# Kernel optimization log

Hardware: AMD Instinct MI355X
Metric: run time of the kernel (lower is better)

The kernel has to match this reference:

```python
import jax, jax.numpy as jnp
import numpy as np

N, E, F_IN, HID, HEADS, OUT, EDIM = 50000, 800000, 128, 64, 2, 40, 5
NEG_SLOPE = 0.2


def setup_inputs() -> dict:
    key = jax.random.key(0)
    ks = jax.random.split(key, 16)
    x = jax.random.normal(ks[0], (N, F_IN), jnp.float32)
    # build edge_index with src != dst so PyG's remove_self_loops is a no-op
    dst = jax.random.randint(ks[1], (E,), 0, N, dtype=jnp.int32)
    off = jax.random.randint(ks[2], (E,), 1, N, dtype=jnp.int32)
    src = (dst + off) % N
    edge_index = jnp.stack([src, dst], axis=0)
    edge_attr = jax.random.normal(ks[3], (E, EDIM), jnp.float32)
    s = 0.1
    params = dict(
        W1=jax.random.normal(ks[4], (F_IN, HEADS * HID), jnp.float32) * s,
        att_src1=jax.random.normal(ks[5], (HEADS, HID), jnp.float32) * s,
        att_dst1=jax.random.normal(ks[6], (HEADS, HID), jnp.float32) * s,
        We1=jax.random.normal(ks[7], (EDIM, HEADS * HID), jnp.float32) * s,
        att_e1=jax.random.normal(ks[8], (HEADS, HID), jnp.float32) * s,
        b1=jnp.zeros((HEADS * HID,), jnp.float32),
        W2=jax.random.normal(ks[9], (HEADS * HID, OUT), jnp.float32) * s,
        att_src2=jax.random.normal(ks[10], (1, OUT), jnp.float32) * s,
        att_dst2=jax.random.normal(ks[11], (1, OUT), jnp.float32) * s,
        We2=jax.random.normal(ks[12], (EDIM, OUT), jnp.float32) * s,
        att_e2=jax.random.normal(ks[13], (1, OUT), jnp.float32) * s,
        b2=jnp.zeros((OUT,), jnp.float32),
    )
    return dict(x=x, edge_index=edge_index, edge_attr=edge_attr, **params)


def _add_self_loops(src, dst, eattr, n):
    # PyG add_self_loops with fill_value='mean': per-dst-node mean of incoming edge_attr
    cnt = jax.ops.segment_sum(jnp.ones_like(dst, jnp.float32), dst, num_segments=n)
    loop_attr = jax.ops.segment_sum(eattr, dst, num_segments=n) / jnp.maximum(cnt, 1.0)[:, None]
    ar = jnp.arange(n, dtype=src.dtype)
    return (jnp.concatenate([src, ar]), jnp.concatenate([dst, ar]),
            jnp.concatenate([eattr, loop_attr], axis=0))


def _gat_conv(x, src, dst, eattr, W, a_src, a_dst, We, a_e, b):
    n = x.shape[0]
    H, C = a_src.shape
    xh = (x @ W).reshape(n, H, C)                      # [N,H,C]
    al_src = jnp.einsum('nhc,hc->nh', xh, a_src)[src]  # [Etot,H]
    al_dst = jnp.einsum('nhc,hc->nh', xh, a_dst)[dst]
    eh = (eattr @ We).reshape(-1, H, C)                # [Etot,H,C]
    al_e = jnp.einsum('ehc,hc->eh', eh, a_e)
    alpha = jax.nn.leaky_relu(al_src + al_dst + al_e, negative_slope=NEG_SLOPE)
    amax = jax.ops.segment_max(alpha, dst, num_segments=n)  # segment-wise softmax over dst
    ex = jnp.exp(alpha - amax[dst])
    denom = jax.ops.segment_sum(ex, dst, num_segments=n)
    alpha = ex / (denom[dst] + 1e-16)
    out = jax.ops.segment_sum(xh[src] * alpha[:, :, None], dst, num_segments=n)
    return out.reshape(n, H * C) + b


def reference(x, edge_index, edge_attr, W1, att_src1, att_dst1, We1, att_e1, b1,
              W2, att_src2, att_dst2, We2, att_e2, b2):
    src, dst = edge_index[0], edge_index[1]
    s2, d2, ea2 = _add_self_loops(src, dst, edge_attr, x.shape[0])
    h = jax.nn.elu(_gat_conv(x, s2, d2, ea2, W1, att_src1, att_dst1, We1, att_e1, b1))
    logits = _gat_conv(h, s2, d2, ea2, W2, att_src2, att_dst2, We2, att_e2, b2)
    return jax.nn.log_softmax(logits, axis=1)
```

## Files before the change

### kernel.cpp

```cpp
#include <hip/hip_runtime.h>
#include <hip/hip_fp16.h>
#include <math.h>

#define N_NODES 50000
#define N_EDGES 800000
#define F_IN    128
#define HID     64
#define HEADS   2
#define C1      128
#define OUT_C   40
#define EDIM    5
#define NEG_SLOPE 0.2f
#define CAPN    64
#define NPB1    16
#define NPB2    8
#define SCAN_B  256
#define SCAN_NB ((N_NODES + SCAN_B - 1) / SCAN_B)

constexpr size_t pad64(size_t n){ return (n + 63) / 64 * 64; }
constexpr size_t O_CNT      = 0;
constexpr size_t O_ZERO_END = O_CNT      + pad64(N_NODES);
constexpr size_t O_RANK     = O_ZERO_END;
constexpr size_t O_ROWPTR   = O_RANK     + pad64(N_EDGES);
constexpr size_t O_STMP     = O_ROWPTR   + pad64(N_NODES+1);
constexpr size_t O_BSUM     = O_STMP     + pad64(N_NODES);
constexpr size_t O_BOFF     = O_BSUM     + pad64(SCAN_NB);
constexpr size_t O_EREC     = O_BOFF     + pad64(SCAN_NB);
constexpr size_t O_WEATT    = O_EREC     + pad64((size_t)N_EDGES*2);
constexpr size_t O_XHB      = O_WEATT    + 64;
constexpr size_t O_AS1      = O_XHB      + pad64((size_t)N_NODES*C1/2);
constexpr size_t O_AD1      = O_AS1      + pad64((size_t)N_NODES*2);
constexpr size_t O_H1       = O_AD1      + pad64((size_t)N_NODES*2);
constexpr size_t O_XH2B     = O_H1       + pad64((size_t)N_NODES*C1);
constexpr size_t O_AS2      = O_XH2B     + pad64((size_t)N_NODES*OUT_C/2);
constexpr size_t O_AD2      = O_AS2      + pad64(N_NODES);

__device__ __forceinline__ float lrelu(float v){ return v >= 0.f ? v : NEG_SLOPE*v; }
__device__ __forceinline__ float bfl(unsigned u){ return __uint_as_float(u << 16); }
__device__ __forceinline__ float bfh(unsigned u){ return __uint_as_float(u & 0xFFFF0000u); }
__device__ __forceinline__ unsigned short f2bf(float f){
  unsigned u = __float_as_uint(f);
  return (unsigned short)((u + 0x7FFFu + ((u >> 16) & 1u)) >> 16);
}
__device__ __forceinline__ unsigned f2h(float f){
  return (unsigned)__half_as_ushort(__float2half(f));
}
__device__ __forceinline__ float h2f(unsigned u){
  return __half2float(__ushort_as_half((unsigned short)(u & 0xFFFFu)));
}

__global__ void k_weatt(const float* __restrict__ We1, const float* __restrict__ ae1,
                        const float* __restrict__ We2, const float* __restrict__ ae2,
                        float* __restrict__ weatt){
  int t = threadIdx.x;
  if (t < 10){
    int k = t >> 1, h = t & 1;
    float s = 0.f;
    for (int c = 0; c < HID; c++) s += We1[k*C1 + h*HID + c] * ae1[h*HID + c];
    weatt[k*2 + h] = s;
  } else if (t < 15){
    int k = t - 10;
    float s = 0.f;
    for (int c = 0; c < OUT_C; c++) s += We2[k*OUT_C + c] * ae2[c];
    weatt[10 + k] = s;
  }
}

__global__ void k_count(const int* __restrict__ dst, int* __restrict__ cnt,
                        int* __restrict__ rank){
  int e = blockIdx.x*blockDim.x + threadIdx.x;
  if (e >= N_EDGES) return;
  rank[e] = atomicAdd(&cnt[dst[e]], 1);
}

__global__ void __launch_bounds__(SCAN_B) k_scan1(const int* __restrict__ cnt,
                                                  int* __restrict__ stmp,
                                                  int* __restrict__ bsum){
  int blk = blockIdx.x, t = threadIdx.x;
  int i = blk*SCAN_B + t;
  int v = (i < N_NODES) ? cnt[i] : 0;
  int lane = t & 63, w = t >> 6;
  int x = v;
  #pragma unroll
  for (int off = 1; off < 64; off <<= 1){
    int y = __shfl_up(x, off);
    if (lane >= off) x += y;
  }
  __shared__ int wsum[SCAN_B/64];
  if (lane == 63) wsum[w] = x;
  __syncthreads();
  int add = 0;
  for (int k = 0; k < w; k++) add += wsum[k];
  x += add;
  if (i < N_NODES) stmp[i] = x;
  if (t == SCAN_B-1) bsum[blk] = x;
}

__global__ void __launch_bounds__(SCAN_B) k_scan2(const int* __restrict__ bsum,
                                                  int* __restrict__ boff){
  int t = threadIdx.x;
  int v = (t < SCAN_NB) ? bsum[t] : 0;
  int lane = t & 63, w = t >> 6;
  int x = v;
  #pragma unroll
  for (int off = 1; off < 64; off <<= 1){
    int y = __shfl_up(x, off);
    if (lane >= off) x += y;
  }
  __shared__ int wsum[SCAN_B/64];
  if (lane == 63) wsum[w] = x;
  __syncthreads();
  int add = 0;
  for (int k = 0; k < w; k++) add += wsum[k];
  x += add;
  if (t < SCAN_NB) boff[t] = x - v;
}

__global__ void __launch_bounds__(SCAN_B) k_scan3(const int* __restrict__ stmp,
                                                  const int* __restrict__ boff,
                                                  int* __restrict__ rowptr){
  int blk = blockIdx.x, t = threadIdx.x;
  int i = blk*SCAN_B + t;
  if (i < N_NODES) rowptr[i+1] = stmp[i] + boff[blk];
  if (i == 0) rowptr[0] = 0;
}

__global__ void k_scatter(const int* __restrict__ src, const int* __restrict__ dst,
                          const int* __restrict__ rank,
                          const float* __restrict__ eattr, const int* __restrict__ rowptr,
                          const float* __restrict__ weatt,
                          uint2* __restrict__ erec){
  int e = blockIdx.x*blockDim.x + threadIdx.x;
  if (e >= N_EDGES) return;
  int d = dst[e];
  int pos = rowptr[d] + rank[e];
  float a[EDIM];
  #pragma unroll
  for (int k = 0; k < EDIM; k++) a[k] = eattr[e*EDIM + k];
  float l0 = 0.f, l1 = 0.f, l2 = 0.f;
  #pragma unroll
  for (int k = 0; k < EDIM; k++){
    l0 += a[k]*weatt[k*2 + 0];
    l1 += a[k]*weatt[k*2 + 1];
    l2 += a[k]*weatt[10 + k];
  }
  unsigned w0 = (unsigned)src[e] | (f2h(l2) << 16);
  unsigned w1 = f2h(l0) | (f2h(l1) << 16);
  erec[pos] = make_uint2(w0, w1);
}

#define T1_ROWS 128
#define T1_KK   32
__global__ void __launch_bounds__(256) k_gemm1(const float* __restrict__ x,
                                               const float* __restrict__ W,
                                               const float* __restrict__ a_src,
                                               const float* __restrict__ a_dst,
                                               unsigned short* __restrict__ xhb,
                                               float* __restrict__ as_o,
                                               float* __restrict__ ad_o){
  __shared__ float xs[T1_ROWS][T1_KK+1];
  __shared__ float ws[T1_KK][C1];
  int tid = threadIdx.x;
  int tx = tid & 15, ty = tid >> 4;
  int r0 = blockIdx.x * T1_ROWS;
  float acc[8][8];
  #pragma unroll
  for (int i = 0; i < 8; i++)
    #pragma unroll
    for (int j = 0; j < 8; j++) acc[i][j] = 0.f;

  for (int kb = 0; kb < F_IN; kb += T1_KK){
    __syncthreads();
    for (int i = tid; i < T1_ROWS*(T1_KK/4); i += 256){
      int r = i >> 3, c4 = (i & 7) * 4;
      int row = r0 + r;
      float4 v = (row < N_NODES) ? *(const float4*)&x[(size_t)row*F_IN + kb + c4]
                                 : make_float4(0.f,0.f,0.f,0.f);
      xs[r][c4+0]=v.x; xs[r][c4+1]=v.y; xs[r][c4+2]=v.z; xs[r][c4+3]=v.w;
    }
    for (int i = tid; i < T1_KK*(C1/4); i += 256){
      int k = i >> 5, c4 = (i & 31) * 4;
      *(float4*)&ws[k][c4] = *(const float4*)&W[(size_t)(kb + k)*C1 + c4];
    }
    __syncthreads();
    #pragma unroll 4
    for (int k = 0; k < T1_KK; k++){
      float a[8], b[8];
      #pragma unroll
      for (int i = 0; i < 8; i++) a[i] = xs[ty*8 + i][k];
      float4 b0 = *(const float4*)&ws[k][tx*8];
      float4 b1 = *(const float4*)&ws[k][tx*8+4];
      b[0]=b0.x; b[1]=b0.y; b[2]=b0.z; b[3]=b0.w;
      b[4]=b1.x; b[5]=b1.y; b[6]=b1.z; b[7]=b1.w;
      #pragma unroll
      for (int i = 0; i < 8; i++)
        #pragma unroll
        for (int j = 0; j < 8; j++)
          acc[i][j] += a[i]*b[j];
    }
  }
  float asv[8], adv[8];
  #pragma unroll
  for (int j = 0; j < 8; j++){
    asv[j] = a_src[tx*8 + j];
    adv[j] = a_dst[tx*8 + j];
  }
  int h = tx >> 3;
  #pragma unroll
  for (int i = 0; i < 8; i++){
    int row = r0 + ty*8 + i;
    bool ok = row < N_NODES;
    if (ok){
      unsigned short hh[8];
      #pragma unroll
      for (int j = 0; j < 8; j++) hh[j] = f2bf(acc[i][j]);
      uint4 pk;
      pk.x = (unsigned)hh[0] | ((unsigned)hh[1] << 16);
      pk.y = (unsigned)hh[2] | ((unsigned)hh[3] << 16);
      pk.z = (unsigned)hh[4] | ((unsigned)hh[5] << 16);
      pk.w = (unsigned)hh[6] | ((unsigned)hh[7] << 16);
      *(uint4*)&xhb[(size_t)row*C1 + tx*8] = pk;
    }
    float s = 0.f, d = 0.f;
    #pragma unroll
    for (int j = 0; j < 8; j++){ s += acc[i][j]*asv[j]; d += acc[i][j]*adv[j]; }
    s += __shfl_xor(s, 1); s += __shfl_xor(s, 2); s += __shfl_xor(s, 4);
    d += __shfl_xor(d, 1); d += __shfl_xor(d, 2); d += __shfl_xor(d, 4);
    if (ok && (tx & 7) == 0){
      as_o[row*2 + h] = s;
      ad_o[row*2 + h] = d;
    }
  }
}

__global__ void __launch_bounds__(256) k_agg1(const unsigned short* __restrict__ xhb,
    const int* __restrict__ rowptr, const uint2* __restrict__ erec,
    const float* __restrict__ as1, const float* __restrict__ ad1,
    const float* __restrict__ b1, float* __restrict__ h1){
  __shared__ float2 eC[NPB1][CAPN+1];
  __shared__ int    sC[NPB1][CAPN+1];
  int t = threadIdx.x;
  int g = t >> 4, l = t & 15;
  int n = blockIdx.x*NPB1 + g;
  if (n >= N_NODES) return;
  int beg = rowptr[n], end = rowptr[n+1];
  int deg = end - beg;
  float2 adn = *(const float2*)&ad1[n*2];
  bool cached = (deg <= CAPN);

  float s0 = 0.f, s1 = 0.f, la0 = 0.f, la1 = 0.f;
  for (int i = l; i < deg; i += 16){
    uint2 r = erec[(size_t)beg + i];
    int s = r.x & 0xFFFFu;
    float al0 = h2f(r.y), al1 = h2f(r.y >> 16);
    float2 a = *(const float2*)&as1[s*2];
    float e0 = expf(lrelu(a.x + adn.x + al0));
    float e1 = expf(lrelu(a.y + adn.y + al1));
    if (cached){ sC[g][i] = s * C1; eC[g][i] = make_float2(e0, e1); }
    s0 += e0; s1 += e1; la0 += al0; la1 += al1;
  }
  #pragma unroll
  for (int off = 1; off < 16; off <<= 1){
    s0 += __shfl_xor(s0, off); s1 += __shfl_xor(s1, off);
    la0 += __shfl_xor(la0, off); la1 += __shfl_xor(la1, off);
  }
  float inv = 1.f / fmaxf((float)deg, 1.f);
  float2 asn = *(const float2*)&as1[n*2];
  float sl0 = lrelu(asn.x + adn.x + la0*inv);
  float sl1 = lrelu(asn.y + adn.y + la1*inv);
  float es0 = expf(sl0), es1 = expf(sl1);
  float S0 = s0 + es0 + 1e-16f;
  float S1 = s1 + es1 + 1e-16f;

  int head = l >> 3;
  float acc[8];
  #pragma unroll
  for (int j = 0; j < 8; j++) acc[j] = 0.f;
  if (cached){
    for (int k = 0; k < deg; k++){
      float2 e2 = eC[g][k];
      float e = head ? e2.y : e2.x;
      uint4 r = *(const uint4*)&xhb[sC[g][k] + l*8];
      acc[0] += e*bfl(r.x); acc[1] += e*bfh(r.x);
      acc[2] += e*bfl(r.y); acc[3] += e*bfh(r.y);
      acc[4] += e*bfl(r.z); acc[5] += e*bfh(r.z);
      acc[6] += e*bfl(r.w); acc[7] += e*bfh(r.w);
    }
  } else {
    for (int k = 0; k < deg; k++){
      uint2 rr = erec[(size_t)beg + k];
      int s = rr.x & 0xFFFFu;
      float2 a = *(const float2*)&as1[s*2];
      float e = head ? expf(lrelu(a.y + adn.y + h2f(rr.y >> 16)))
                     : expf(lrelu(a.x + adn.x + h2f(rr.y)));
      uint4 r = *(const uint4*)&xhb[(size_t)s*C1 + l*8];
      acc[0] += e*bfl(r.x); acc[1] += e*bfh(r.x);
      acc[2] += e*bfl(r.y); acc[3] += e*bfh(r.y);
      acc[4] += e*bfl(r.z); acc[5] += e*bfh(r.z);
      acc[6] += e*bfl(r.w); acc[7] += e*bfh(r.w);
    }
  }
  float es = head ? es1 : es0;
  float den = head ? S1 : S0;
  uint4 r = *(const uint4*)&xhb[(size_t)n*C1 + l*8];
  float xs8[8];
  xs8[0]=bfl(r.x); xs8[1]=bfh(r.x); xs8[2]=bfl(r.y); xs8[3]=bfh(r.y);
  xs8[4]=bfl(r.z); xs8[5]=bfh(r.z); xs8[6]=bfl(r.w); xs8[7]=bfh(r.w);
  float o[8];
  #pragma unroll
  for (int j = 0; j < 8; j++){
    float v = (acc[j] + es*xs8[j]) / den + b1[l*8 + j];
    o[j] = v > 0.f ? v : expm1f(v);
  }
  *(float4*)&h1[(size_t)n*C1 + l*8]     = make_float4(o[0],o[1],o[2],o[3]);
  *(float4*)&h1[(size_t)n*C1 + l*8 + 4] = make_float4(o[4],o[5],o[6],o[7]);
}

#define T2_ROWS 128
#define T2_KK   32
__global__ void __launch_bounds__(256) k_gemm2(const float* __restrict__ h1,
    const float* __restrict__ W2, const float* __restrict__ a_src2,
    const float* __restrict__ a_dst2,
    unsigned short* __restrict__ xh2b, float* __restrict__ as_o, float* __restrict__ ad_o){
  __shared__ float hs[T2_ROWS][T2_KK+1];
  __shared__ float ws[F_IN*OUT_C];
  int tid = threadIdx.x;
  int tx = tid & 7, ty = tid >> 3;
  int r0 = blockIdx.x * T2_ROWS;
  for (int i = tid; i < F_IN*OUT_C/4; i += 256)
    ((float4*)ws)[i] = ((const float4*)W2)[i];
  float acc[4][5];
  #pragma unroll
  for (int i = 0; i < 4; i++)
    #pragma unroll
    for (int j = 0; j < 5; j++) acc[i][j] = 0.f;

  for (int kb = 0; kb < F_IN; kb += T2_KK){
    __syncthreads();
    for (int i = tid; i < T2_ROWS*(T2_KK/4); i += 256){
      int r = i >> 3, c4 = (i & 7) * 4;
      int row = r0 + r;
      float4 v = (row < N_NODES) ? *(const float4*)&h1[(size_t)row*F_IN + kb + c4]
                                 : make_float4(0.f,0.f,0.f,0.f);
      hs[r][c4+0]=v.x; hs[r][c4+1]=v.y; hs[r][c4+2]=v.z; hs[r][c4+3]=v.w;
    }
    __syncthreads();
    #pragma unroll 4
    for (int k = 0; k < T2_KK; k++){
      float a[4], b[5];
      #pragma unroll
      for (int i = 0; i < 4; i++) a[i] = hs[ty*4 + i][k];
      #pragma unroll
      for (int j = 0; j < 5; j++) b[j] = ws[(kb + k)*OUT_C + tx*5 + j];
      #pragma unroll
      for (int i = 0; i < 4; i++)
        #pragma unroll
        for (int j = 0; j < 5; j++)
          acc[i][j] += a[i]*b[j];
    }
  }
  float asv[5], adv[5];
  #pragma unroll
  for (int j = 0; j < 5; j++){
    asv[j] = a_src2[tx*5 + j];
    adv[j] = a_dst2[tx*5 + j];
  }
  #pragma unroll
  for (int i = 0; i < 4; i++){
    int row = r0 + ty*4 + i;
    bool ok = row < N_NODES;
    if (ok){
      #pragma unroll
      for (int j = 0; j < 5; j++)
        xh2b[(size_t)row*OUT_C + tx*5 + j] = f2bf(acc[i][j]);
    }
    float s = 0.f, d = 0.f;
    #pragma unroll
    for (int j = 0; j < 5; j++){ s += acc[i][j]*asv[j]; d += acc[i][j]*adv[j]; }
    s += __shfl_xor(s, 1); s += __shfl_xor(s, 2); s += __shfl_xor(s, 4);
    d += __shfl_xor(d, 1); d += __shfl_xor(d, 2); d += __shfl_xor(d, 4);
    if (ok && tx == 0){
      as_o[row] = s;
      ad_o[row] = d;
    }
  }
}

__global__ void __launch_bounds__(256) k_agg2(const unsigned short* __restrict__ xh2b,
    const int* __restrict__ rowptr, const uint2* __restrict__ erec,
    const float* __restrict__ as2, const float* __restrict__ ad2,
    const float* __restrict__ b2, float* __restrict__ out){
  __shared__ float eC[NPB2][CAPN+1];
  __shared__ int   sC[NPB2][CAPN+1];
  int t = threadIdx.x;
  int g = t >> 5, l = t & 31;
  int n = blockIdx.x*NPB2 + g;
  if (n >= N_NODES) return;
  int beg = rowptr[n], end = rowptr[n+1];
  int deg = end - beg;
  float adv = ad2[n];
  bool cached = (deg <= CAPN);

  float ss = 0.f, la = 0.f;
  for (int i = l; i < deg; i += 32){
    uint2 r = erec[(size_t)beg + i];
    int s = r.x & 0xFFFFu;
    float al2 = h2f(r.x >> 16);
    float e = expf(lrelu(as2[s] + adv + al2));
    if (cached){ sC[g][i] = s * OUT_C; eC[g][i] = e; }
    ss += e; la += al2;
  }
  #pragma unroll
  for (int off = 1; off < 32; off <<= 1){
    ss += __shfl_xor(ss, off);
    la += __shfl_xor(la, off);
  }
  float inv = 1.f / fmaxf((float)deg, 1.f);
  float sl = lrelu(as2[n] + adv + la*inv);
  float es = expf(sl);
  float S = ss + es + 1e-16f;

  float a0 = 0.f, a1 = 0.f;
  if (l < 20){
    if (cached){
      for (int k = 0; k < deg; k++){
        float e = eC[g][k];
        unsigned u = *(const unsigned*)&xh2b[sC[g][k] + l*2];
        a0 += e*bfl(u); a1 += e*bfh(u);
      }
    } else {
      for (int k = 0; k < deg; k++){
        uint2 rr = erec[(size_t)beg + k];
        int s = rr.x & 0xFFFFu;
        float e = expf(lrelu(as2[s] + adv + h2f(rr.x >> 16)));
        unsigned u = *(const unsigned*)&xh2b[(size_t)s*OUT_C + l*2];
        a0 += e*bfl(u); a1 += e*bfh(u);
      }
    }
  }
  float o0 = -INFINITY, o1 = -INFINITY;
  if (l < 20){
    unsigned u = *(const unsigned*)&xh2b[(size_t)n*OUT_C + l*2];
    o0 = (a0 + es*bfl(u)) / S + b2[l*2 + 0];
    o1 = (a1 + es*bfh(u)) / S + b2[l*2 + 1];
  }
  float mm = fmaxf(o0, o1);
  #pragma unroll
  for (int off = 1; off < 32; off <<= 1) mm = fmaxf(mm, __shfl_xor(mm, off));
  float e = (l < 20) ? (expf(o0 - mm) + expf(o1 - mm)) : 0.f;
  #pragma unroll
  for (int off = 1; off < 32; off <<= 1) e += __shfl_xor(e, off);
  if (l < 20){
    float lse = logf(e);
    out[(size_t)n*OUT_C + l*2 + 0] = o0 - mm - lse;
    out[(size_t)n*OUT_C + l*2 + 1] = o1 - mm - lse;
  }
}

extern "C" void kernel_launch(void* const* d_in, const int* in_sizes, int n_in,
                              void* d_out, int out_size, void* d_ws, size_t ws_size,
                              hipStream_t stream){
  const float* x        = (const float*)d_in[0];
  const int*   ei       = (const int*)  d_in[1];
  const float* eattr    = (const float*)d_in[2];
  const float* W1       = (const float*)d_in[3];
  const float* att_src1 = (const float*)d_in[4];
  const float* att_dst1 = (const float*)d_in[5];
  const float* We1      = (const float*)d_in[6];
  const float* att_e1   = (const float*)d_in[7];
  const float* b1       = (const float*)d_in[8];
  const float* W2       = (const float*)d_in[9];
  const float* att_src2 = (const float*)d_in[10];
  const float* att_dst2 = (const float*)d_in[11];
  const float* We2      = (const float*)d_in[12];
  const float* att_e2   = (const float*)d_in[13];
  const float* b2       = (const float*)d_in[14];
  const int* src = ei;
  const int* dst = ei + N_EDGES;

  float* wsf    = (float*)d_ws;
  int*   cnt     = (int*)(wsf + O_CNT);
  int*   rank    = (int*)(wsf + O_RANK);
  int*   rowptr  = (int*)(wsf + O_ROWPTR);
  int*   stmp    = (int*)(wsf + O_STMP);
  int*   bsum    = (int*)(wsf + O_BSUM);
  int*   boff    = (int*)(wsf + O_BOFF);
  uint2* erec    = (uint2*)(wsf + O_EREC);
  float* weatt   = wsf + O_WEATT;
  unsigned short* xhb  = (unsigned short*)(wsf + O_XHB);
  float* as1     = wsf + O_AS1;
  float* ad1     = wsf + O_AD1;
  float* h1      = wsf + O_H1;
  unsigned short* xh2b = (unsigned short*)(wsf + O_XH2B);
  float* as2     = wsf + O_AS2;
  float* ad2     = wsf + O_AD2;
  float* out     = (float*)d_out;

  hipMemsetAsync(wsf + O_CNT, 0, O_ZERO_END*sizeof(float), stream);

  const int EB = (N_EDGES + 255) / 256;

  k_weatt  <<<1, 64, 0, stream>>>(We1, att_e1, We2, att_e2, weatt);
  k_count  <<<EB, 256, 0, stream>>>(dst, cnt, rank);
  k_scan1  <<<SCAN_NB, SCAN_B, 0, stream>>>(cnt, stmp, bsum);
  k_scan2  <<<1, SCAN_B, 0, stream>>>(bsum, boff);
  k_scan3  <<<SCAN_NB, SCAN_B, 0, stream>>>(stmp, boff, rowptr);
  k_scatter<<<EB, 256, 0, stream>>>(src, dst, rank, eattr, rowptr, weatt, erec);

  k_gemm1  <<<(N_NODES + T1_ROWS - 1)/T1_ROWS, 256, 0, stream>>>(x, W1, att_src1, att_dst1,
                                                                 xhb, as1, ad1);
  k_agg1   <<<(N_NODES + NPB1 - 1)/NPB1, 256, 0, stream>>>(xhb, rowptr, erec, as1, ad1, b1, h1);

  k_gemm2  <<<(N_NODES + T2_ROWS - 1)/T2_ROWS, 256, 0, stream>>>(h1, W2, att_src2, att_dst2,
                                                                 xh2b, as2, ad2);
  k_agg2   <<<(N_NODES + NPB2 - 1)/NPB2, 256, 0, stream>>>(xh2b, rowptr, erec, as2, ad2, b2, out);
}
```

Before: 190.6 us.

## Rewrite first-layer GEMM with bf16 MFMA and fold weatt into scan2

Replaces the FP32 register-tiled x@W1 kernel with a bf16 MFMA 16x16x32 kernel. Each block transposes all of W1 into LDS as bf16, each wave computes a 16x128 tile, and results are staged through LDS to pack bf16 output and compute the attention dot products. Separately, the tiny edge-attention weight precompute is merged into the single-block scan2 kernel to drop one launch. Converting x and W to bf16 before the multiply lowers accuracy relative to the FP32 accumulate path. Every block also re-converts the full 128x128 W1 into LDS.

```diff
diff --git a/kernel.cpp b/kernel.cpp
--- a/kernel.cpp
+++ b/kernel.cpp
@@ -16,6 +16,9 @@
 #define NPB2    8
 #define SCAN_B  256
 #define SCAN_NB ((N_NODES + SCAN_B - 1) / SCAN_B)
+
+typedef __bf16 bf16x8 __attribute__((ext_vector_type(8)));
+typedef float  f32x4v __attribute__((ext_vector_type(4)));
 
 constexpr size_t pad64(size_t n){ return (n + 63) / 64 * 64; }
 constexpr size_t O_CNT      = 0;
@@ -49,10 +52,59 @@
   return __half2float(__ushort_as_half((unsigned short)(u & 0xFFFFu)));
 }
 
-__global__ void k_weatt(const float* __restrict__ We1, const float* __restrict__ ae1,
-                        const float* __restrict__ We2, const float* __restrict__ ae2,
-                        float* __restrict__ weatt){
+__global__ void k_count(const int* __restrict__ dst, int* __restrict__ cnt,
+                        int* __restrict__ rank){
+  int e = blockIdx.x*blockDim.x + threadIdx.x;
+  if (e >= N_EDGES) return;
+  rank[e] = atomicAdd(&cnt[dst[e]], 1);
+}
+
+__global__ void __launch_bounds__(SCAN_B) k_scan1(const int* __restrict__ cnt,
+                                                  int* __restrict__ stmp,
+                                                  int* __restrict__ bsum){
+  int blk = blockIdx.x, t = threadIdx.x;
+  int i = blk*SCAN_B + t;
+  int v = (i < N_NODES) ? cnt[i] : 0;
+  int lane = t & 63, w = t >> 6;
+  int x = v;
+  #pragma unroll
+  for (int off = 1; off < 64; off <<= 1){
+    int y = __shfl_up(x, off);
+    if (lane >= off) x += y;
+  }
+  __shared__ int wsum[SCAN_B/64];
+  if (lane == 63) wsum[w] = x;
+  __syncthreads();
+  int add = 0;
+  for (int k = 0; k < w; k++) add += wsum[k];
+  x += add;
+  if (i < N_NODES) stmp[i] = x;
+  if (t == SCAN_B-1) bsum[blk] = x;
+}
+
+__global__ void __launch_bounds__(SCAN_B) k_scan2(const int* __restrict__ bsum,
+                                                  int* __restrict__ boff,
+                                                  const float* __restrict__ We1,
+                                                  const float* __restrict__ ae1,
+                                                  const float* __restrict__ We2,
+                                                  const float* __restrict__ ae2,
+                                                  float* __restrict__ weatt){
   int t = threadIdx.x;
+  int v = (t < SCAN_NB) ? bsum[t] : 0;
+  int lane = t & 63, w = t >> 6;
+  int x = v;
+  #pragma unroll
+  for (int off = 1; off < 64; off <<= 1){
+    int y = __shfl_up(x, off);
+    if (lane >= off) x += y;
+  }
+  __shared__ int wsum[SCAN_B/64];
+  if (lane == 63) wsum[w] = x;
+  __syncthreads();
+  int add = 0;
+  for (int k = 0; k < w; k++) add += wsum[k];
+  x += add;
+  if (t < SCAN_NB) boff[t] = x - v;
   if (t < 10){
     int k = t >> 1, h = t & 1;
     float s = 0.f;
@@ -66,56 +118,6 @@
   }
 }
 
-__global__ void k_count(const int* __restrict__ dst, int* __restrict__ cnt,
-                        int* __restrict__ rank){
-  int e = blockIdx.x*blockDim.x + threadIdx.x;
-  if (e >= N_EDGES) return;
-  rank[e] = atomicAdd(&cnt[dst[e]], 1);
-}
-
-__global__ void __launch_bounds__(SCAN_B) k_scan1(const int* __restrict__ cnt,
-                                                  int* __restrict__ stmp,
-                                                  int* __restrict__ bsum){
-  int blk = blockIdx.x, t = threadIdx.x;
-  int i = blk*SCAN_B + t;
-  int v = (i < N_NODES) ? cnt[i] : 0;
-  int lane = t & 63, w = t >> 6;
-  int x = v;
-  #pragma unroll
-  for (int off = 1; off < 64; off <<= 1){
-    int y = __shfl_up(x, off);
-    if (lane >= off) x += y;
-  }
-  __shared__ int wsum[SCAN_B/64];
-  if (lane == 63) wsum[w] = x;
-  __syncthreads();
-  int add = 0;
-  for (int k = 0; k < w; k++) add += wsum[k];
-  x += add;
-  if (i < N_NODES) stmp[i] = x;
-  if (t == SCAN_B-1) bsum[blk] = x;
-}
-
-__global__ void __launch_bounds__(SCAN_B) k_scan2(const int* __restrict__ bsum,
-                                                  int* __restrict__ boff){
-  int t = threadIdx.x;
-  int v = (t < SCAN_NB) ? bsum[t] : 0;
-  int lane = t & 63, w = t >> 6;
-  int x = v;
-  #pragma unroll
-  for (int off = 1; off < 64; off <<= 1){
-    int y = __shfl_up(x, off);
-    if (lane >= off) x += y;
-  }
-  __shared__ int wsum[SCAN_B/64];
-  if (lane == 63) wsum[w] = x;
-  __syncthreads();
-  int add = 0;
-  for (int k = 0; k < w; k++) add += wsum[k];
-  x += add;
-  if (t < SCAN_NB) boff[t] = x - v;
-}
-
 __global__ void __launch_bounds__(SCAN_B) k_scan3(const int* __restrict__ stmp,
                                                   const int* __restrict__ boff,
                                                   int* __restrict__ rowptr){
@@ -149,8 +151,6 @@
   erec[pos] = make_uint2(w0, w1);
 }
 
-#define T1_ROWS 128
-#define T1_KK   32
 __global__ void __launch_bounds__(256) k_gemm1(const float* __restrict__ x,
                                                const float* __restrict__ W,
                                                const float* __restrict__ a_src,
@@ -158,78 +158,83 @@
                                                unsigned short* __restrict__ xhb,
                                                float* __restrict__ as_o,
                                                float* __restrict__ ad_o){
-  __shared__ float xs[T1_ROWS][T1_KK+1];
-  __shared__ float ws[T1_KK][C1];
+  __shared__ __align__(16) unsigned char smem[128*136*2];
+  __bf16 (*wt)[136] = (__bf16(*)[136])smem;
+  float  (*eps)[132] = (float(*)[132])smem;
   int tid = threadIdx.x;
-  int tx = tid & 15, ty = tid >> 4;
-  int r0 = blockIdx.x * T1_ROWS;
-  float acc[8][8];
-  #pragma unroll
-  for (int i = 0; i < 8; i++)
+  int wv = tid >> 6, L = tid & 63;
+  int g = L >> 4, c16 = L & 15;
+  int r0 = blockIdx.x * 64;
+
+  for (int i = tid; i < F_IN*C1; i += 256){
+    int k = i >> 7, c = i & 127;
+    wt[c][k] = (__bf16)W[i];
+  }
+  __syncthreads();
+
+  f32x4v acc[8];
+  #pragma unroll
+  for (int ct = 0; ct < 8; ct++) acc[ct] = (f32x4v){0.f, 0.f, 0.f, 0.f};
+
+  int arow = r0 + wv*16 + c16;
+  bool aok = arow < N_NODES;
+  const float* xrow = &x[(size_t)arow*F_IN];
+  #pragma unroll
+  for (int ks = 0; ks < 4; ks++){
+    int k0 = ks*32 + g*8;
+    bf16x8 a;
+    if (aok){
+      float4 v0 = *(const float4*)&xrow[k0];
+      float4 v1 = *(const float4*)&xrow[k0 + 4];
+      a[0]=(__bf16)v0.x; a[1]=(__bf16)v0.y; a[2]=(__bf16)v0.z; a[3]=(__bf16)v0.w;
+      a[4]=(__bf16)v1.x; a[5]=(__bf16)v1.y; a[6]=(__bf16)v1.z; a[7]=(__bf16)v1.w;
+    } else {
+      a = (bf16x8)(__bf16)0.f;
+    }
     #pragma unroll
-    for (int j = 0; j < 8; j++) acc[i][j] = 0.f;
-
-  for (int kb = 0; kb < F_IN; kb += T1_KK){
-    __syncthreads();
-    for (int i = tid; i < T1_ROWS*(T1_KK/4); i += 256){
-      int r = i >> 3, c4 = (i & 7) * 4;
-      int row = r0 + r;
-      float4 v = (row < N_NODES) ? *(const float4*)&x[(size_t)row*F_IN + kb + c4]
-                                 : make_float4(0.f,0.f,0.f,0.f);
-      xs[r][c4+0]=v.x; xs[r][c4+1]=v.y; xs[r][c4+2]=v.z; xs[r][c4+3]=v.w;
-    }
-    for (int i = tid; i < T1_KK*(C1/4); i += 256){
-      int k = i >> 5, c4 = (i & 31) * 4;
-      *(float4*)&ws[k][c4] = *(const float4*)&W[(size_t)(kb + k)*C1 + c4];
-    }
-    __syncthreads();
-    #pragma unroll 4
-    for (int k = 0; k < T1_KK; k++){
-      float a[8], b[8];
-      #pragma unroll
-      for (int i = 0; i < 8; i++) a[i] = xs[ty*8 + i][k];
-      float4 b0 = *(const float4*)&ws[k][tx*8];
-      float4 b1 = *(const float4*)&ws[k][tx*8+4];
-      b[0]=b0.x; b[1]=b0.y; b[2]=b0.z; b[3]=b0.w;
-      b[4]=b1.x; b[5]=b1.y; b[6]=b1.z; b[7]=b1.w;
-      #pragma unroll
-      for (int i = 0; i < 8; i++)
-        #pragma unroll
-        for (int j = 0; j < 8; j++)
-          acc[i][j] += a[i]*b[j];
-    }
-  }
-  float asv[8], adv[8];
-  #pragma unroll
-  for (int j = 0; j < 8; j++){
-    asv[j] = a_src[tx*8 + j];
-    adv[j] = a_dst[tx*8 + j];
-  }
-  int h = tx >> 3;
-  #pragma unroll
-  for (int i = 0; i < 8; i++){
-    int row = r0 + ty*8 + i;
-    bool ok = row < N_NODES;
-    if (ok){
-      unsigned short hh[8];
-      #pragma unroll
-      for (int j = 0; j < 8; j++) hh[j] = f2bf(acc[i][j]);
-      uint4 pk;
-      pk.x = (unsigned)hh[0] | ((unsigned)hh[1] << 16);
-      pk.y = (unsigned)hh[2] | ((unsigned)hh[3] << 16);
-      pk.z = (unsigned)hh[4] | ((unsigned)hh[5] << 16);
-      pk.w = (unsigned)hh[6] | ((unsigned)hh[7] << 16);
-      *(uint4*)&xhb[(size_t)row*C1 + tx*8] = pk;
-    }
-    float s = 0.f, d = 0.f;
+    for (int ct = 0; ct < 8; ct++){
+      bf16x8 b = *(const bf16x8*)&wt[ct*16 + c16][k0];
+      acc[ct] = __builtin_amdgcn_mfma_f32_16x16x32_bf16(a, b, acc[ct], 0, 0, 0);
+    }
+  }
+  __syncthreads();
+
+  #pragma unroll
+  for (int ct = 0; ct < 8; ct++){
     #pragma unroll
-    for (int j = 0; j < 8; j++){ s += acc[i][j]*asv[j]; d += acc[i][j]*adv[j]; }
-    s += __shfl_xor(s, 1); s += __shfl_xor(s, 2); s += __shfl_xor(s, 4);
-    d += __shfl_xor(d, 1); d += __shfl_xor(d, 2); d += __shfl_xor(d, 4);
-    if (ok && (tx & 7) == 0){
-      as_o[row*2 + h] = s;
-      ad_o[row*2 + h] = d;
-    }
+    for (int r = 0; r < 4; r++)
+      eps[wv*16 + g*4 + r][ct*16 + c16] = acc[ct][r];
+  }
+  __syncthreads();
+
+  int row = tid >> 2, cb = tid & 3;
+  int grow = r0 + row;
+  float vals[32];
+  #pragma unroll
+  for (int j = 0; j < 32; j++) vals[j] = eps[row][cb*32 + j];
+  if (grow < N_NODES){
+    unsigned pk[16];
+    #pragma unroll
+    for (int j = 0; j < 16; j++)
+      pk[j] = (unsigned)f2bf(vals[2*j]) | ((unsigned)f2bf(vals[2*j+1]) << 16);
+    uint4* d4 = (uint4*)&xhb[(size_t)grow*C1 + cb*32];
+    d4[0] = make_uint4(pk[0],pk[1],pk[2],pk[3]);
+    d4[1] = make_uint4(pk[4],pk[5],pk[6],pk[7]);
+    d4[2] = make_uint4(pk[8],pk[9],pk[10],pk[11]);
+    d4[3] = make_uint4(pk[12],pk[13],pk[14],pk[15]);
+  }
+  float s = 0.f, d = 0.f;
+  #pragma unroll
+  for (int j = 0; j < 32; j++){
+    s += vals[j]*a_src[cb*32 + j];
+    d += vals[j]*a_dst[cb*32 + j];
+  }
+  s += __shfl_xor(s, 1);
+  d += __shfl_xor(d, 1);
+  if ((cb & 1) == 0 && grow < N_NODES){
+    int h = cb >> 1;
+    as_o[grow*2 + h] = s;
+    ad_o[grow*2 + h] = d;
   }
 }
 
@@ -500,15 +505,13 @@
 
   const int EB = (N_EDGES + 255) / 256;
 
-  k_weatt  <<<1, 64, 0, stream>>>(We1, att_e1, We2, att_e2, weatt);
   k_count  <<<EB, 256, 0, stream>>>(dst, cnt, rank);
   k_scan1  <<<SCAN_NB, SCAN_B, 0, stream>>>(cnt, stmp, bsum);
-  k_scan2  <<<1, SCAN_B, 0, stream>>>(bsum, boff);
+  k_scan2  <<<1, SCAN_B, 0, stream>>>(bsum, boff, We1, att_e1, We2, att_e2, weatt);
   k_scan3  <<<SCAN_NB, SCAN_B, 0, stream>>>(stmp, boff, rowptr);
   k_scatter<<<EB, 256, 0, stream>>>(src, dst, rank, eattr, rowptr, weatt, erec);
 
-  k_gemm1  <<<(N_NODES + T1_ROWS - 1)/T1_ROWS, 256, 0, stream>>>(x, W1, att_src1, att_dst1,
-                                                                 xhb, as1, ad1);
+  k_gemm1  <<<(N_NODES + 63)/64, 256, 0, stream>>>(x, W1, att_src1, att_dst1, xhb, as1, ad1);
   k_agg1   <<<(N_NODES + NPB1 - 1)/NPB1, 256, 0, stream>>>(xhb, rowptr, erec, as1, ad1, b1, h1);
 
   k_gemm2  <<<(N_NODES + T2_ROWS - 1)/T2_ROWS, 256, 0, stream>>>(h1, W2, att_src2, att_dst2,
```

Measured after the change: 179.1 us. -6.0%, faster.
